# Optimization experiments

Hardware: AMD Instinct MI355X
Metric: run time of the kernel (lower is better)

Reference implementation:

```python
import jax, jax.numpy as jnp
import numpy as np


def setup_inputs() -> dict:
    key = jax.random.key(0)
    k1, k2 = jax.random.split(key)
    B, T, D = 16, 1024, 256
    z = jax.random.normal(k1, (B, T, D), dtype=jnp.float32)
    gt_dT = jax.random.normal(k2, (B, T, T, 4), dtype=jnp.float32)
    sigma = jnp.full((4,), 0.1, dtype=jnp.float32)
    return {"z": z, "gt_dT": gt_dT, "sigma": sigma}


def reference(z, gt_dT, sigma):
    # z: [B,T,D], gt_dT: [B,T,T,4], sigma: [4]
    B, T, D = z.shape
    # Gaussian kernel over pairwise displacements -> w: [B,T,T]
    inv2s2 = 1.0 / (2.0 * sigma * sigma)  # [4]
    kernel = jnp.einsum('btsk,k->bts', gt_dT * gt_dT, inv2s2)
    w = jnp.exp(-kernel)  # [B,T,T]

    z2 = jnp.sum(z * z, axis=-1)          # [B,T]
    w_col_sum = jnp.sum(w, axis=2)        # [B,T]
    term1 = jnp.sum(z2 * w_col_sum, axis=1)  # [B]

    wz = jnp.einsum('bts,bsd->btd', w, z)    # [B,T,D]
    term2 = jnp.sum(wz * z, axis=(1, 2))     # [B]

    w_row_sum = jnp.sum(w, axis=1)           # [B,T]
    term3 = jnp.sum(z2 * w_row_sum, axis=1)  # [B]

    loss = jnp.mean(term1 - 2.0 * term2 + term3) / (T * T)
    return loss
```

## Files before the change

kernel.cpp:

```cpp
#include <hip/hip_runtime.h>
#include <hip/hip_bf16.h>
#include <stdint.h>

#define BB 16
#define TT 1024
#define DD 256

typedef __attribute__((ext_vector_type(8))) short short8;
typedef __attribute__((ext_vector_type(4))) float floatx4;

__device__ __forceinline__ unsigned short f2bf(float f) {
    union { float f; unsigned int u; } c; c.f = f;
    unsigned int u = c.u;
    unsigned int r = (u + 0x7FFFu + ((u >> 16) & 1u)) >> 16;
    return (unsigned short)r;
}

__global__ __launch_bounds__(256) void prep_kernel(
    const float* __restrict__ z, float* __restrict__ z2,
    unsigned short* __restrict__ zb, double* __restrict__ acc) {
    if (blockIdx.x == 0 && threadIdx.x == 0) *acc = 0.0;
    const int lane = threadIdx.x & 63;
    const int row  = blockIdx.x * 4 + (threadIdx.x >> 6);
    const float4 v = ((const float4*)(z + (size_t)row * DD))[lane];
    float ss = v.x * v.x + v.y * v.y + v.z * v.z + v.w * v.w;
    ushort4 o;
    o.x = f2bf(v.x); o.y = f2bf(v.y); o.z = f2bf(v.z); o.w = f2bf(v.w);
    ((ushort4*)(zb + (size_t)row * DD))[lane] = o;
#pragma unroll
    for (int off = 32; off > 0; off >>= 1) ss += __shfl_down(ss, off);
    if (lane == 0) z2[row] = ss;
}

__global__ __launch_bounds__(256) void patch_kernel(
    const unsigned short* __restrict__ zb, const float* __restrict__ z2,
    const float* __restrict__ gt, const float* __restrict__ sigma,
    double* __restrict__ acc) {
    const float LOG2E = 1.4426950408889634f;
    const float s0v = sigma[0], s1v = sigma[1], s2v = sigma[2], s3v = sigma[3];
    const float nc0 = -LOG2E * 0.5f / (s0v * s0v);
    const float nc1 = -LOG2E * 0.5f / (s1v * s1v);
    const float nc2 = -LOG2E * 0.5f / (s2v * s2v);
    const float nc3 = -LOG2E * 0.5f / (s3v * s3v);

    const int tid  = threadIdx.x;
    const int lane = tid & 63;
    const int quad = lane >> 4;
    const int m    = lane & 15;
    const int wid  = blockIdx.x * 4 + (tid >> 6);

    const int b   = wid >> 10;
    const int rem = wid & 1023;
    const int t0  = (rem >> 5) << 5;
    const int s0  = (rem & 31) << 5;

    const float* gtb = gt + (size_t)b * TT * TT * 4;
    const int    tq  = t0 + quad * 4;

    float4 gtv[16];
#pragma unroll
    for (int r = 0; r < 4; ++r) {
        const size_t row0 = (size_t)(tq + r) * TT;
        const size_t row1 = (size_t)(tq + 16 + r) * TT;
        gtv[r * 4 + 0] = *(const float4*)(gtb + (row0 + (s0 + m)) * 4);
        gtv[r * 4 + 1] = *(const float4*)(gtb + (row0 + (s0 + 16 + m)) * 4);
        gtv[r * 4 + 2] = *(const float4*)(gtb + (row1 + (s0 + m)) * 4);
        gtv[r * 4 + 3] = *(const float4*)(gtb + (row1 + (s0 + 16 + m)) * 4);
    }

    const unsigned short* zrow = zb + (size_t)b * TT * DD;
    const short8* at0 = (const short8*)(zrow + (t0 + m) * DD + quad * 8);
    const short8* at1 = (const short8*)(zrow + (t0 + 16 + m) * DD + quad * 8);
    const short8* bs0 = (const short8*)(zrow + (s0 + m) * DD + quad * 8);
    const short8* bs1 = (const short8*)(zrow + (s0 + 16 + m) * DD + quad * 8);

    floatx4 g00 = {0.f, 0.f, 0.f, 0.f};
    floatx4 g01 = {0.f, 0.f, 0.f, 0.f};
    floatx4 g10 = {0.f, 0.f, 0.f, 0.f};
    floatx4 g11 = {0.f, 0.f, 0.f, 0.f};
#pragma unroll
    for (int k = 0; k < 8; ++k) {
        const short8 a0 = at0[k * 4];
        const short8 a1 = at1[k * 4];
        const short8 b0 = bs0[k * 4];
        const short8 b1 = bs1[k * 4];
        g00 = __builtin_amdgcn_mfma_f32_16x16x32_bf16(a0, b0, g00, 0, 0, 0);
        g01 = __builtin_amdgcn_mfma_f32_16x16x32_bf16(a0, b1, g01, 0, 0, 0);
        g10 = __builtin_amdgcn_mfma_f32_16x16x32_bf16(a1, b0, g10, 0, 0, 0);
        g11 = __builtin_amdgcn_mfma_f32_16x16x32_bf16(a1, b1, g11, 0, 0, 0);
    }

    const float* z2b  = z2 + b * TT;
    const float  z2s0 = z2b[s0 + m];
    const float  z2s1 = z2b[s0 + 16 + m];

    float partial = 0.f;
#pragma unroll
    for (int r = 0; r < 4; ++r) {
        const float z2t0 = z2b[tq + r];
        const float z2t1 = z2b[tq + 16 + r];
        const float e00 = z2t0 + z2s0, e01 = z2t0 + z2s1;
        const float e10 = z2t1 + z2s0, e11 = z2t1 + z2s1;
        {
            const float4 d = gtv[r * 4 + 0];
            const float k2 = fmaf(nc3, d.w * d.w, fmaf(nc2, d.z * d.z,
                             fmaf(nc1, d.y * d.y, nc0 * d.x * d.x)));
            partial = fmaf(exp2f(k2), fmaf(-2.f, g00[r], e00), partial);
        }
        {
            const float4 d = gtv[r * 4 + 1];
            const float k2 = fmaf(nc3, d.w * d.w, fmaf(nc2, d.z * d.z,
                             fmaf(nc1, d.y * d.y, nc0 * d.x * d.x)));
            partial = fmaf(exp2f(k2), fmaf(-2.f, g01[r], e01), partial);
        }
        {
            const float4 d = gtv[r * 4 + 2];
            const float k2 = fmaf(nc3, d.w * d.w, fmaf(nc2, d.z * d.z,
                             fmaf(nc1, d.y * d.y, nc0 * d.x * d.x)));
            partial = fmaf(exp2f(k2), fmaf(-2.f, g10[r], e10), partial);
        }
        {
            const float4 d = gtv[r * 4 + 3];
            const float k2 = fmaf(nc3, d.w * d.w, fmaf(nc2, d.z * d.z,
                             fmaf(nc1, d.y * d.y, nc0 * d.x * d.x)));
            partial = fmaf(exp2f(k2), fmaf(-2.f, g11[r], e11), partial);
        }
    }

#pragma unroll
    for (int off = 32; off > 0; off >>= 1) partial += __shfl_down(partial, off);
    __shared__ float red[4];
    if (lane == 0) red[tid >> 6] = partial;
    __syncthreads();
    if (tid == 0) atomicAdd(acc, (double)(red[0] + red[1] + red[2] + red[3]));
}

__global__ void finalize_kernel(const double* __restrict__ acc, float* __restrict__ out) {
    out[0] = (float)(*acc * (1.0 / ((double)BB * (double)TT * (double)TT)));
}

extern "C" void kernel_launch(void* const* d_in, const int* in_sizes, int n_in,
                              void* d_out, int out_size, void* d_ws, size_t ws_size,
                              hipStream_t stream) {
    const float* z     = (const float*)d_in[0];
    const float* gt    = (const float*)d_in[1];
    const float* sigma = (const float*)d_in[2];
    float* out = (float*)d_out;

    char* ws = (char*)d_ws;
    double* acc        = (double*)ws;
    float* z2          = (float*)(ws + 64);
    unsigned short* zb = (unsigned short*)(ws + 64 + (size_t)BB * TT * sizeof(float));

    prep_kernel<<<BB * TT / 4, 256, 0, stream>>>(z, z2, zb, acc);
    patch_kernel<<<BB * (TT / 32) * (TT / 32) / 4, 256, 0, stream>>>(zb, z2, gt, sigma, acc);
    finalize_kernel<<<1, 1, 0, stream>>>(acc, out);
}
```

Baseline: 402.4 us.

## Use nontemporal split gt loads and spread atomic accumulation over 64 slots

The gt displacement loads become nontemporal, and they are split into two halves so the second half is fetched after the MFMA work, which cuts live registers from 16 to 8 float4s. The single double atomic accumulator becomes 64 slots indexed by block, and a 64-thread finalize kernel reduces them, to cut atomic contention on one address. The risks are less memory-level parallelism from the split loads, and the second-half loads being serialized behind the first-half compute.

```diff
diff --git a/kernel.cpp b/kernel.cpp
--- a/kernel.cpp
+++ b/kernel.cpp
@@ -5,9 +5,11 @@
 #define BB 16
 #define TT 1024
 #define DD 256
+#define NACC 64
 
 typedef __attribute__((ext_vector_type(8))) short short8;
 typedef __attribute__((ext_vector_type(4))) float floatx4;
+typedef __attribute__((ext_vector_type(4))) float fvec4;
 
 __device__ __forceinline__ unsigned short f2bf(float f) {
     union { float f; unsigned int u; } c; c.f = f;
@@ -19,7 +21,7 @@
 __global__ __launch_bounds__(256) void prep_kernel(
     const float* __restrict__ z, float* __restrict__ z2,
     unsigned short* __restrict__ zb, double* __restrict__ acc) {
-    if (blockIdx.x == 0 && threadIdx.x == 0) *acc = 0.0;
+    if (blockIdx.x == 0 && threadIdx.x < NACC) acc[threadIdx.x] = 0.0;
     const int lane = threadIdx.x & 63;
     const int row  = blockIdx.x * 4 + (threadIdx.x >> 6);
     const float4 v = ((const float4*)(z + (size_t)row * DD))[lane];
@@ -57,15 +59,15 @@
     const float* gtb = gt + (size_t)b * TT * TT * 4;
     const int    tq  = t0 + quad * 4;
 
-    float4 gtv[16];
+    fvec4 gtv[8];
 #pragma unroll
-    for (int r = 0; r < 4; ++r) {
+    for (int r = 0; r < 2; ++r) {
         const size_t row0 = (size_t)(tq + r) * TT;
         const size_t row1 = (size_t)(tq + 16 + r) * TT;
-        gtv[r * 4 + 0] = *(const float4*)(gtb + (row0 + (s0 + m)) * 4);
-        gtv[r * 4 + 1] = *(const float4*)(gtb + (row0 + (s0 + 16 + m)) * 4);
-        gtv[r * 4 + 2] = *(const float4*)(gtb + (row1 + (s0 + m)) * 4);
-        gtv[r * 4 + 3] = *(const float4*)(gtb + (row1 + (s0 + 16 + m)) * 4);
+        gtv[r * 4 + 0] = __builtin_nontemporal_load((const fvec4*)(gtb + (row0 + (s0 + m)) * 4));
+        gtv[r * 4 + 1] = __builtin_nontemporal_load((const fvec4*)(gtb + (row0 + (s0 + 16 + m)) * 4));
+        gtv[r * 4 + 2] = __builtin_nontemporal_load((const fvec4*)(gtb + (row1 + (s0 + m)) * 4));
+        gtv[r * 4 + 3] = __builtin_nontemporal_load((const fvec4*)(gtb + (row1 + (s0 + 16 + m)) * 4));
     }
 
     const unsigned short* zrow = zb + (size_t)b * TT * DD;
@@ -95,35 +97,51 @@
     const float  z2s1 = z2b[s0 + 16 + m];
 
     float partial = 0.f;
+
 #pragma unroll
-    for (int r = 0; r < 4; ++r) {
-        const float z2t0 = z2b[tq + r];
-        const float z2t1 = z2b[tq + 16 + r];
-        const float e00 = z2t0 + z2s0, e01 = z2t0 + z2s1;
-        const float e10 = z2t1 + z2s0, e11 = z2t1 + z2s1;
-        {
-            const float4 d = gtv[r * 4 + 0];
-            const float k2 = fmaf(nc3, d.w * d.w, fmaf(nc2, d.z * d.z,
-                             fmaf(nc1, d.y * d.y, nc0 * d.x * d.x)));
-            partial = fmaf(exp2f(k2), fmaf(-2.f, g00[r], e00), partial);
+    for (int half = 0; half < 2; ++half) {
+        if (half == 1) {
+#pragma unroll
+            for (int r = 0; r < 2; ++r) {
+                const size_t row0 = (size_t)(tq + 2 + r) * TT;
+                const size_t row1 = (size_t)(tq + 18 + r) * TT;
+                gtv[r * 4 + 0] = __builtin_nontemporal_load((const fvec4*)(gtb + (row0 + (s0 + m)) * 4));
+                gtv[r * 4 + 1] = __builtin_nontemporal_load((const fvec4*)(gtb + (row0 + (s0 + 16 + m)) * 4));
+                gtv[r * 4 + 2] = __builtin_nontemporal_load((const fvec4*)(gtb + (row1 + (s0 + m)) * 4));
+                gtv[r * 4 + 3] = __builtin_nontemporal_load((const fvec4*)(gtb + (row1 + (s0 + 16 + m)) * 4));
+            }
         }
-        {
-            const float4 d = gtv[r * 4 + 1];
-            const float k2 = fmaf(nc3, d.w * d.w, fmaf(nc2, d.z * d.z,
-                             fmaf(nc1, d.y * d.y, nc0 * d.x * d.x)));
-            partial = fmaf(exp2f(k2), fmaf(-2.f, g01[r], e01), partial);
-        }
-        {
-            const float4 d = gtv[r * 4 + 2];
-            const float k2 = fmaf(nc3, d.w * d.w, fmaf(nc2, d.z * d.z,
-                             fmaf(nc1, d.y * d.y, nc0 * d.x * d.x)));
-            partial = fmaf(exp2f(k2), fmaf(-2.f, g10[r], e10), partial);
-        }
-        {
-            const float4 d = gtv[r * 4 + 3];
-            const float k2 = fmaf(nc3, d.w * d.w, fmaf(nc2, d.z * d.z,
-                             fmaf(nc1, d.y * d.y, nc0 * d.x * d.x)));
-            partial = fmaf(exp2f(k2), fmaf(-2.f, g11[r], e11), partial);
+#pragma unroll
+        for (int r = 0; r < 2; ++r) {
+            const int rr = half * 2 + r;
+            const float z2t0 = z2b[tq + rr];
+            const float z2t1 = z2b[tq + 16 + rr];
+            const float e00 = z2t0 + z2s0, e01 = z2t0 + z2s1;
+            const float e10 = z2t1 + z2s0, e11 = z2t1 + z2s1;
+            {
+                const fvec4 d = gtv[r * 4 + 0];
+                const float k2 = fmaf(nc3, d.w * d.w, fmaf(nc2, d.z * d.z,
+                                 fmaf(nc1, d.y * d.y, nc0 * d.x * d.x)));
+                partial = fmaf(exp2f(k2), fmaf(-2.f, g00[rr], e00), partial);
+            }
+            {
+                const fvec4 d = gtv[r * 4 + 1];
+                const float k2 = fmaf(nc3, d.w * d.w, fmaf(nc2, d.z * d.z,
+                                 fmaf(nc1, d.y * d.y, nc0 * d.x * d.x)));
+                partial = fmaf(exp2f(k2), fmaf(-2.f, g01[rr], e01), partial);
+            }
+            {
+                const fvec4 d = gtv[r * 4 + 2];
+                const float k2 = fmaf(nc3, d.w * d.w, fmaf(nc2, d.z * d.z,
+                                 fmaf(nc1, d.y * d.y, nc0 * d.x * d.x)));
+                partial = fmaf(exp2f(k2), fmaf(-2.f, g10[rr], e10), partial);
+            }
+            {
+                const fvec4 d = gtv[r * 4 + 3];
+                const float k2 = fmaf(nc3, d.w * d.w, fmaf(nc2, d.z * d.z,
+                                 fmaf(nc1, d.y * d.y, nc0 * d.x * d.x)));
+                partial = fmaf(exp2f(k2), fmaf(-2.f, g11[rr], e11), partial);
+            }
         }
     }
 
@@ -132,11 +150,17 @@
     __shared__ float red[4];
     if (lane == 0) red[tid >> 6] = partial;
     __syncthreads();
-    if (tid == 0) atomicAdd(acc, (double)(red[0] + red[1] + red[2] + red[3]));
+    if (tid == 0)
+        atomicAdd(&acc[blockIdx.x & (NACC - 1)],
+                  (double)(red[0] + red[1] + red[2] + red[3]));
 }
 
 __global__ void finalize_kernel(const double* __restrict__ acc, float* __restrict__ out) {
-    out[0] = (float)(*acc * (1.0 / ((double)BB * (double)TT * (double)TT)));
+    double v = acc[threadIdx.x];
+#pragma unroll
+    for (int off = 32; off > 0; off >>= 1) v += __shfl_down(v, off);
+    if (threadIdx.x == 0)
+        out[0] = (float)(v * (1.0 / ((double)BB * (double)TT * (double)TT)));
 }
 
 extern "C" void kernel_launch(void* const* d_in, const int* in_sizes, int n_in,
@@ -149,10 +173,10 @@
 
     char* ws = (char*)d_ws;
     double* acc        = (double*)ws;
-    float* z2          = (float*)(ws + 64);
-    unsigned short* zb = (unsigned short*)(ws + 64 + (size_t)BB * TT * sizeof(float));
+    float* z2          = (float*)(ws + 512);
+    unsigned short* zb = (unsigned short*)(ws + 512 + (size_t)BB * TT * sizeof(float));
 
     prep_kernel<<<BB * TT / 4, 256, 0, stream>>>(z, z2, zb, acc);
     patch_kernel<<<BB * (TT / 32) * (TT / 32) / 4, 256, 0, stream>>>(zb, z2, gt, sigma, acc);
-    finalize_kernel<<<1, 1, 0, stream>>>(acc, out);
+    finalize_kernel<<<1, 64, 0, stream>>>(acc, out);
 }
```

New measurement: 386.2 us. -4.0%, faster.

## Widen per-wave tile, double-buffer gt loads, fuse finalize via last-block reduction

Applied to the files above, without the earlier changes.

Each wave now covers a 32x64 tile instead of 32x32, which reuses the A operand across twice as many MFMAs. The gt_dT loads are split into half-tiles that are software-pipelined against the exp epilogue, and they use nontemporal loads. The single global double atomic is spread over 64 slots, and a last-block counter performs the final reduction, so the separate finalize kernel launch goes away. In exchange the kernel holds more accumulator registers, which may lower occupancy, and it adds threadfence/counter logic.

```diff
diff --git a/kernel.cpp b/kernel.cpp
--- a/kernel.cpp
+++ b/kernel.cpp
@@ -5,9 +5,11 @@
 #define BB 16
 #define TT 1024
 #define DD 256
+#define NACC 64
 
 typedef __attribute__((ext_vector_type(8))) short short8;
 typedef __attribute__((ext_vector_type(4))) float floatx4;
+typedef __attribute__((ext_vector_type(4))) float fvec4;
 
 __device__ __forceinline__ unsigned short f2bf(float f) {
     union { float f; unsigned int u; } c; c.f = f;
@@ -18,8 +20,12 @@
 
 __global__ __launch_bounds__(256) void prep_kernel(
     const float* __restrict__ z, float* __restrict__ z2,
-    unsigned short* __restrict__ zb, double* __restrict__ acc) {
-    if (blockIdx.x == 0 && threadIdx.x == 0) *acc = 0.0;
+    unsigned short* __restrict__ zb, double* __restrict__ acc,
+    unsigned int* __restrict__ cnt) {
+    if (blockIdx.x == 0) {
+        if (threadIdx.x < NACC) acc[threadIdx.x] = 0.0;
+        if (threadIdx.x == NACC) *cnt = 0u;
+    }
     const int lane = threadIdx.x & 63;
     const int row  = blockIdx.x * 4 + (threadIdx.x >> 6);
     const float4 v = ((const float4*)(z + (size_t)row * DD))[lane];
@@ -35,7 +41,8 @@
 __global__ __launch_bounds__(256) void patch_kernel(
     const unsigned short* __restrict__ zb, const float* __restrict__ z2,
     const float* __restrict__ gt, const float* __restrict__ sigma,
-    double* __restrict__ acc) {
+    double* __restrict__ acc, unsigned int* __restrict__ cnt,
+    float* __restrict__ out) {
     const float LOG2E = 1.4426950408889634f;
     const float s0v = sigma[0], s1v = sigma[1], s2v = sigma[2], s3v = sigma[3];
     const float nc0 = -LOG2E * 0.5f / (s0v * s0v);
@@ -49,94 +56,129 @@
     const int m    = lane & 15;
     const int wid  = blockIdx.x * 4 + (tid >> 6);
 
-    const int b   = wid >> 10;
-    const int rem = wid & 1023;
-    const int t0  = (rem >> 5) << 5;
-    const int s0  = (rem & 31) << 5;
+    const int b   = wid >> 9;
+    const int rem = wid & 511;
+    const int t0  = (rem >> 4) << 5;
+    const int s0  = (rem & 15) << 6;
 
     const float* gtb = gt + (size_t)b * TT * TT * 4;
     const int    tq  = t0 + quad * 4;
 
-    float4 gtv[16];
-#pragma unroll
-    for (int r = 0; r < 4; ++r) {
-        const size_t row0 = (size_t)(tq + r) * TT;
-        const size_t row1 = (size_t)(tq + 16 + r) * TT;
-        gtv[r * 4 + 0] = *(const float4*)(gtb + (row0 + (s0 + m)) * 4);
-        gtv[r * 4 + 1] = *(const float4*)(gtb + (row0 + (s0 + 16 + m)) * 4);
-        gtv[r * 4 + 2] = *(const float4*)(gtb + (row1 + (s0 + m)) * 4);
-        gtv[r * 4 + 3] = *(const float4*)(gtb + (row1 + (s0 + 16 + m)) * 4);
+    fvec4 gtv[8];
+#define GT_LOAD(dst, colbase)                                                   \
+    {                                                                           \
+        _Pragma("unroll")                                                       \
+        for (int r = 0; r < 2; ++r) {                                           \
+            const size_t row0 = (size_t)(tq + rrbase + r) * TT;                 \
+            const size_t row1 = (size_t)(tq + 16 + rrbase + r) * TT;            \
+            dst[r * 4 + 0] = __builtin_nontemporal_load((const fvec4*)(gtb + (row0 + (colbase) + m) * 4));        \
+            dst[r * 4 + 1] = __builtin_nontemporal_load((const fvec4*)(gtb + (row0 + (colbase) + 16 + m) * 4));   \
+            dst[r * 4 + 2] = __builtin_nontemporal_load((const fvec4*)(gtb + (row1 + (colbase) + m) * 4));        \
+            dst[r * 4 + 3] = __builtin_nontemporal_load((const fvec4*)(gtb + (row1 + (colbase) + 16 + m) * 4));   \
+        }                                                                       \
+    }
+    {
+        const int rrbase = 0;
+        GT_LOAD(gtv, s0)
     }
 
     const unsigned short* zrow = zb + (size_t)b * TT * DD;
-    const short8* at0 = (const short8*)(zrow + (t0 + m) * DD + quad * 8);
-    const short8* at1 = (const short8*)(zrow + (t0 + 16 + m) * DD + quad * 8);
-    const short8* bs0 = (const short8*)(zrow + (s0 + m) * DD + quad * 8);
-    const short8* bs1 = (const short8*)(zrow + (s0 + 16 + m) * DD + quad * 8);
-
-    floatx4 g00 = {0.f, 0.f, 0.f, 0.f};
-    floatx4 g01 = {0.f, 0.f, 0.f, 0.f};
-    floatx4 g10 = {0.f, 0.f, 0.f, 0.f};
-    floatx4 g11 = {0.f, 0.f, 0.f, 0.f};
+    const short8* at0  = (const short8*)(zrow + (t0 + m) * DD + quad * 8);
+    const short8* at1  = (const short8*)(zrow + (t0 + 16 + m) * DD + quad * 8);
+    const short8* bsA0 = (const short8*)(zrow + (s0 + m) * DD + quad * 8);
+    const short8* bsA1 = (const short8*)(zrow + (s0 + 16 + m) * DD + quad * 8);
+    const short8* bsB0 = (const short8*)(zrow + (s0 + 32 + m) * DD + quad * 8);
+    const short8* bsB1 = (const short8*)(zrow + (s0 + 48 + m) * DD + quad * 8);
+
+    floatx4 gA00 = {0.f,0.f,0.f,0.f}, gA01 = {0.f,0.f,0.f,0.f};
+    floatx4 gA10 = {0.f,0.f,0.f,0.f}, gA11 = {0.f,0.f,0.f,0.f};
+    floatx4 gB00 = {0.f,0.f,0.f,0.f}, gB01 = {0.f,0.f,0.f,0.f};
+    floatx4 gB10 = {0.f,0.f,0.f,0.f}, gB11 = {0.f,0.f,0.f,0.f};
 #pragma unroll
     for (int k = 0; k < 8; ++k) {
         const short8 a0 = at0[k * 4];
         const short8 a1 = at1[k * 4];
-        const short8 b0 = bs0[k * 4];
-        const short8 b1 = bs1[k * 4];
-        g00 = __builtin_amdgcn_mfma_f32_16x16x32_bf16(a0, b0, g00, 0, 0, 0);
-        g01 = __builtin_amdgcn_mfma_f32_16x16x32_bf16(a0, b1, g01, 0, 0, 0);
-        g10 = __builtin_amdgcn_mfma_f32_16x16x32_bf16(a1, b0, g10, 0, 0, 0);
-        g11 = __builtin_amdgcn_mfma_f32_16x16x32_bf16(a1, b1, g11, 0, 0, 0);
-    }
-
-    const float* z2b  = z2 + b * TT;
-    const float  z2s0 = z2b[s0 + m];
-    const float  z2s1 = z2b[s0 + 16 + m];
+        const short8 b0 = bsA0[k * 4];
+        const short8 b1 = bsA1[k * 4];
+        const short8 b2 = bsB0[k * 4];
+        const short8 b3 = bsB1[k * 4];
+        gA00 = __builtin_amdgcn_mfma_f32_16x16x32_bf16(a0, b0, gA00, 0, 0, 0);
+        gA01 = __builtin_amdgcn_mfma_f32_16x16x32_bf16(a0, b1, gA01, 0, 0, 0);
+        gA10 = __builtin_amdgcn_mfma_f32_16x16x32_bf16(a1, b0, gA10, 0, 0, 0);
+        gA11 = __builtin_amdgcn_mfma_f32_16x16x32_bf16(a1, b1, gA11, 0, 0, 0);
+        gB00 = __builtin_amdgcn_mfma_f32_16x16x32_bf16(a0, b2, gB00, 0, 0, 0);
+        gB01 = __builtin_amdgcn_mfma_f32_16x16x32_bf16(a0, b3, gB01, 0, 0, 0);
+        gB10 = __builtin_amdgcn_mfma_f32_16x16x32_bf16(a1, b2, gB10, 0, 0, 0);
+        gB11 = __builtin_amdgcn_mfma_f32_16x16x32_bf16(a1, b3, gB11, 0, 0, 0);
+    }
+
+    const float* z2b   = z2 + b * TT;
+    const float  z2sA0 = z2b[s0 + m];
+    const float  z2sA1 = z2b[s0 + 16 + m];
+    const float  z2sB0 = z2b[s0 + 32 + m];
+    const float  z2sB1 = z2b[s0 + 48 + m];
 
     float partial = 0.f;
-#pragma unroll
-    for (int r = 0; r < 4; ++r) {
-        const float z2t0 = z2b[tq + r];
-        const float z2t1 = z2b[tq + 16 + r];
-        const float e00 = z2t0 + z2s0, e01 = z2t0 + z2s1;
-        const float e10 = z2t1 + z2s0, e11 = z2t1 + z2s1;
-        {
-            const float4 d = gtv[r * 4 + 0];
-            const float k2 = fmaf(nc3, d.w * d.w, fmaf(nc2, d.z * d.z,
-                             fmaf(nc1, d.y * d.y, nc0 * d.x * d.x)));
-            partial = fmaf(exp2f(k2), fmaf(-2.f, g00[r], e00), partial);
-        }
-        {
-            const float4 d = gtv[r * 4 + 1];
-            const float k2 = fmaf(nc3, d.w * d.w, fmaf(nc2, d.z * d.z,
-                             fmaf(nc1, d.y * d.y, nc0 * d.x * d.x)));
-            partial = fmaf(exp2f(k2), fmaf(-2.f, g01[r], e01), partial);
-        }
-        {
-            const float4 d = gtv[r * 4 + 2];
-            const float k2 = fmaf(nc3, d.w * d.w, fmaf(nc2, d.z * d.z,
-                             fmaf(nc1, d.y * d.y, nc0 * d.x * d.x)));
-            partial = fmaf(exp2f(k2), fmaf(-2.f, g10[r], e10), partial);
-        }
-        {
-            const float4 d = gtv[r * 4 + 3];
-            const float k2 = fmaf(nc3, d.w * d.w, fmaf(nc2, d.z * d.z,
-                             fmaf(nc1, d.y * d.y, nc0 * d.x * d.x)));
-            partial = fmaf(exp2f(k2), fmaf(-2.f, g11[r], e11), partial);
-        }
-    }
+    fvec4 gtn[8];
+
+#define EPILOGUE(src, rrbase, G00, G01, G10, G11, Z2S0, Z2S1)                   \
+    {                                                                           \
+        _Pragma("unroll")                                                       \
+        for (int r = 0; r < 2; ++r) {                                           \
+            const int rr = rrbase + r;                                          \
+            const float z2t0 = z2b[tq + rr];                                    \
+            const float z2t1 = z2b[tq + 16 + rr];                               \
+            const float e00 = z2t0 + Z2S0, e01 = z2t0 + Z2S1;                   \
+            const float e10 = z2t1 + Z2S0, e11 = z2t1 + Z2S1;                   \
+            fvec4 d;                                                            \
+            d = src[r * 4 + 0];                                                 \
+            partial = fmaf(exp2f(fmaf(nc3, d.w * d.w, fmaf(nc2, d.z * d.z,      \
+                      fmaf(nc1, d.y * d.y, nc0 * d.x * d.x)))),                 \
+                      fmaf(-2.f, G00[rr], e00), partial);                       \
+            d = src[r * 4 + 1];                                                 \
+            partial = fmaf(exp2f(fmaf(nc3, d.w * d.w, fmaf(nc2, d.z * d.z,      \
+                      fmaf(nc1, d.y * d.y, nc0 * d.x * d.x)))),                 \
+                      fmaf(-2.f, G01[rr], e01), partial);                       \
+            d = src[r * 4 + 2];                                                 \
+            partial = fmaf(exp2f(fmaf(nc3, d.w * d.w, fmaf(nc2, d.z * d.z,      \
+                      fmaf(nc1, d.y * d.y, nc0 * d.x * d.x)))),                 \
+                      fmaf(-2.f, G10[rr], e10), partial);                       \
+            d = src[r * 4 + 3];                                                 \
+            partial = fmaf(exp2f(fmaf(nc3, d.w * d.w, fmaf(nc2, d.z * d.z,      \
+                      fmaf(nc1, d.y * d.y, nc0 * d.x * d.x)))),                 \
+                      fmaf(-2.f, G11[rr], e11), partial);                       \
+        }                                                                       \
+    }
+
+    { const int rrbase = 2; GT_LOAD(gtn, s0) }
+    EPILOGUE(gtv, 0, gA00, gA01, gA10, gA11, z2sA0, z2sA1)
+    { const int rrbase = 0; GT_LOAD(gtv, s0 + 32) }
+    EPILOGUE(gtn, 2, gA00, gA01, gA10, gA11, z2sA0, z2sA1)
+    { const int rrbase = 2; GT_LOAD(gtn, s0 + 32) }
+    EPILOGUE(gtv, 0, gB00, gB01, gB10, gB11, z2sB0, z2sB1)
+    EPILOGUE(gtn, 2, gB00, gB01, gB10, gB11, z2sB0, z2sB1)
 
 #pragma unroll
     for (int off = 32; off > 0; off >>= 1) partial += __shfl_down(partial, off);
     __shared__ float red[4];
+    __shared__ int is_last;
     if (lane == 0) red[tid >> 6] = partial;
     __syncthreads();
-    if (tid == 0) atomicAdd(acc, (double)(red[0] + red[1] + red[2] + red[3]));
-}
-
-__global__ void finalize_kernel(const double* __restrict__ acc, float* __restrict__ out) {
-    out[0] = (float)(*acc * (1.0 / ((double)BB * (double)TT * (double)TT)));
+    if (tid == 0) {
+        atomicAdd(&acc[blockIdx.x & (NACC - 1)],
+                  (double)(red[0] + red[1] + red[2] + red[3]));
+        __threadfence();
+        const unsigned int done = atomicAdd(cnt, 1u);
+        is_last = (done == gridDim.x - 1) ? 1 : 0;
+    }
+    __syncthreads();
+    if (is_last && tid < NACC) {
+        double v = atomicAdd(&acc[tid], 0.0);
+#pragma unroll
+        for (int off = 32; off > 0; off >>= 1) v += __shfl_down(v, off);
+        if (tid == 0)
+            out[0] = (float)(v * (1.0 / ((double)BB * (double)TT * (double)TT)));
+    }
 }
 
 extern "C" void kernel_launch(void* const* d_in, const int* in_sizes, int n_in,
@@ -149,10 +191,10 @@
 
     char* ws = (char*)d_ws;
     double* acc        = (double*)ws;
-    float* z2          = (float*)(ws + 64);
-    unsigned short* zb = (unsigned short*)(ws + 64 + (size_t)BB * TT * sizeof(float));
-
-    prep_kernel<<<BB * TT / 4, 256, 0, stream>>>(z, z2, zb, acc);
-    patch_kernel<<<BB * (TT / 32) * (TT / 32) / 4, 256, 0, stream>>>(zb, z2, gt, sigma, acc);
-    finalize_kernel<<<1, 1, 0, stream>>>(acc, out);
-}
+    unsigned int* cnt  = (unsigned int*)(ws + 512);
+    float* z2          = (float*)(ws + 1024);
+    unsigned short* zb = (unsigned short*)(ws + 1024 + (size_t)BB * TT * sizeof(float));
+
+    prep_kernel<<<BB * TT / 4, 256, 0, stream>>>(z, z2, zb, acc, cnt);
+    patch_kernel<<<BB * (TT / 32) * (TT / 64) / 4, 256, 0, stream>>>(zb, z2, gt, sigma, acc, cnt, out);
+}
```

Result: slower. 472.3 us (+17.4%).
